# Performance work log

Hardware: AMD Instinct MI355X
Metric: run time of the kernel (lower is better)

Reference implementation:

```python
import jax, jax.numpy as jnp
import numpy as np

LOG2PI = float(np.log(2.0 * np.pi))
EPS_SHIFT = -0.5   # self.eps
TAU = 0.5          # self.tau
ETA = 1.0          # self.eta
MAG_A = 5500.0     # magnitude remap constants from forward()
MAG_B = 1100.0


def setup_inputs() -> dict:
    key = jax.random.key(0)
    k1, k2, k3, k4, k5 = jax.random.split(key, 5)
    B, K, C = 4096, 128, 64
    z = jax.random.normal(k1, (B, K, 2), dtype=jnp.float32)
    # per-keypoint mixture weights summing to 1 (GMM weights_)
    weights = jax.nn.softmax(jax.random.normal(k2, (K, C), dtype=jnp.float32), axis=-1)
    means = jax.random.normal(k3, (K, C, 2), dtype=jnp.float32)
    # SPD covariances: A A^T + 0.2 I
    A = jax.random.normal(k4, (K, C, 2, 2), dtype=jnp.float32) * 0.3
    covs = jnp.einsum('kcij,kclj->kcil', A, A) + 0.2 * jnp.eye(2, dtype=jnp.float32)
    # latent_stats unnormalization factor per latent coordinate (2/(max-min))
    scale = jax.random.uniform(k5, (K, 2), dtype=jnp.float32, minval=0.5, maxval=2.0)
    return {"z": z, "weights": weights, "means": means, "covs": covs, "scale": scale}


def _gmm_pdf_and_grad(z, weights, means, covs):
    # z: [B,K,2]  weights: [K,C]  means: [K,C,2]  covs: [K,C,2,2]
    a = covs[..., 0, 0]; b = covs[..., 0, 1]
    c = covs[..., 1, 0]; d = covs[..., 1, 1]
    det = a * d - b * c                                  # [K,C]
    inv00 = d / det; inv01 = -b / det
    inv10 = -c / det; inv11 = a / det
    diff = z[:, :, None, :] - means[None]                # [B,K,C,2]
    d0 = diff[..., 0]; d1 = diff[..., 1]
    s0 = inv00 * d0 + inv01 * d1                         # Sigma^{-1} diff, [B,K,C]
    s1 = inv10 * d0 + inv11 * d1
    maha = d0 * s0 + d1 * s1                             # [B,K,C]
    logp = -0.5 * (maha + jnp.log(det) + 2.0 * LOG2PI)   # MVN log_prob (D=2)
    comp = weights[None] * jnp.exp(logp)                 # weighted component densities
    pdf = comp.sum(-1)                                   # [B,K]
    # analytic grad of pdf wrt z: sum_c comp_c * (-Sigma_c^{-1} (z-mu_c))
    g0 = -(comp * s0).sum(-1)
    g1 = -(comp * s1).sum(-1)
    grad = jnp.stack([g0, g1], axis=-1)                  # [B,K,2]
    return pdf, grad


def reference(z, weights, means, covs, scale):
    B, K, _ = z.shape
    pdf, grad = _gmm_pdf_and_grad(z, weights, means, covs)
    # densities duplicated per coordinate: [pdf_i, pdf_i] per keypoint -> [B, 2K]
    densities = jnp.repeat(pdf, 2, axis=-1)
    density_norm = jax.nn.sigmoid((densities + EPS_SHIFT) / TAU)
    # unnormalize_gradient: elementwise rescale into raw latent space
    grad_raw = grad * scale[None]                        # [B,K,2]
    nrm = jnp.linalg.norm(grad_raw, axis=-1, keepdims=True)  # [B,K,1]
    mag = jnp.exp((-nrm + MAG_A) / MAG_B)
    negexp_grad = (grad_raw / nrm) * mag                 # [B,K,2]
    return density_norm, ETA * negexp_grad.reshape(B, 2 * K)
```

## Files before the change

### kernel.cpp

```cpp
#include <hip/hip_runtime.h>

#define K_KP   128
#define C_COMP 64
#define TK     8
#define TBS    32
#define NB     4
#define LDS_STRIDE 388

typedef float v2f __attribute__((ext_vector_type(2)));

#if __has_builtin(__builtin_amdgcn_exp2f)
#define EXP2F(x) __builtin_amdgcn_exp2f(x)
#else
#define EXP2F(x) exp2f(x)
#endif
#if __has_builtin(__builtin_amdgcn_logf)
#define LOG2F_(x) __builtin_amdgcn_logf(x)
#else
#define LOG2F_(x) __log2f(x)
#endif
#if __has_builtin(__builtin_amdgcn_rcpf)
#define RCPF(x) __builtin_amdgcn_rcpf(x)
#else
#define RCPF(x) (1.0f/(x))
#endif
#if __has_builtin(__builtin_amdgcn_rsqf)
#define RSQF(x) __builtin_amdgcn_rsqf(x)
#else
#define RSQF(x) rsqrtf(x)
#endif

#define EVAL(m0, m1, i00, i01, i11, lc, ZX, ZY, PDF, G0, G1)            \
    {                                                                   \
        v2f d0 = ZX - (m0);                                             \
        v2f d1 = ZY - (m1);                                             \
        v2f s0 = (i00) * d0 + (i01) * d1;   \
        v2f s1 = (i01) * d0 + (i11) * d1;                               \
        v2f arg = (lc) - d0 * s0 - d1 * s1;           \
        v2f e;                                                          \
        e.x = EXP2F(arg.x);                                             \
        e.y = EXP2F(arg.y);                                             \
        PDF += e;                                                       \
        G0 += e * s0;                                                   \
        G1 += e * s1;                                                   \
    }

__global__ __launch_bounds__(256, 4) void recovery_kernel(
    const float* __restrict__ z,
    const float* __restrict__ weights,
    const float* __restrict__ means,
    const float* __restrict__ covs,
    const float* __restrict__ scale,
    float* __restrict__ out, int B)
{
    __shared__ float lds[TK * LDS_STRIDE];

    const int t  = threadIdx.x;
    const int kb = blockIdx.x & 15;
    const int bb = blockIdx.x >> 4;
    const int k0 = kb * TK;
    const int b0 = bb * (TBS * NB);

    const float K2       = 0.72134752044f;
    const float LOG2_2PI = 2.6514961295f;
    for (int i = t; i < TK * C_COMP; i += 256) {
        int kl = i >> 6;
        int c  = i & 63;
        int g  = (k0 + kl) * C_COMP + c;
        float w  = weights[g];
        float m0 = means[2*g], m1 = means[2*g + 1];
        float a  = covs[4*g],     bq = covs[4*g + 1];
        float cq = covs[4*g + 2], d  = covs[4*g + 3];
        float det  = a*d - bq*cq;
        float rdet = RCPF(det);
        float i00 = d  * rdet * K2;
        float i01 = -bq * rdet * K2;
        float i11 = a  * rdet * K2;
        float lc = LOG2F_(w) - LOG2_2PI - 0.5f * LOG2F_(det);
        float* row = &lds[kl * LDS_STRIDE + (c >> 1) * 12];
        ((float4*)(row + (c & 1) * 4))[0] = make_float4(m0, m1, i00, i01);
        ((float2*)(row + 8 + (c & 1) * 2))[0] = make_float2(i11, lc);
    }
    __syncthreads();

    const int kl = t & 7;
    const int bl = t >> 3;
    const int kg = k0 + kl;

    const float2* z2 = (const float2*)z;
    float zx[NB], zy[NB];
#pragma unroll
    for (int j = 0; j < NB; ++j) {
        int b = b0 + bl + j * TBS;
        float2 v = z2[(size_t)b * K_KP + kg];
        zx[j] = v.x; zy[j] = v.y;
    }

    v2f ZXa = {zx[0], zx[1]}, ZXb = {zx[2], zx[3]};
    v2f ZYa = {zy[0], zy[1]}, ZYb = {zy[2], zy[3]};
    v2f pdfa = {0.f, 0.f}, pdfb = {0.f, 0.f};
    v2f g0a  = {0.f, 0.f}, g0b  = {0.f, 0.f};
    v2f g1a  = {0.f, 0.f}, g1b  = {0.f, 0.f};

    const float* kp = &lds[kl * LDS_STRIDE];
#pragma unroll 4
    for (int p = 0; p < C_COMP / 2; ++p) {
        float4 A0 = *(const float4*)(kp + p * 12);
        float4 A1 = *(const float4*)(kp + p * 12 + 4);
        float4 Bp = *(const float4*)(kp + p * 12 + 8);
        EVAL(A0.x, A0.y, A0.z, A0.w, Bp.x, Bp.y, ZXa, ZYa, pdfa, g0a, g1a);
        EVAL(A0.x, A0.y, A0.z, A0.w, Bp.x, Bp.y, ZXb, ZYb, pdfb, g0b, g1b);
        EVAL(A1.x, A1.y, A1.z, A1.w, Bp.z, Bp.w, ZXa, ZYa, pdfa, g0a, g1a);
        EVAL(A1.x, A1.y, A1.z, A1.w, Bp.z, Bp.w, ZXb, ZYb, pdfb, g0b, g1b);
    }

    float pdf[NB] = {pdfa.x, pdfa.y, pdfb.x, pdfb.y};
    float gs0[NB] = {g0a.x, g0a.y, g0b.x, g0b.y};
    float gs1[NB] = {g1a.x, g1a.y, g1b.x, g1b.y};

    float2 sc = ((const float2*)scale)[kg];
    const float NEG_INV_K2 = -1.3862943611f;
    float f0 = sc.x * NEG_INV_K2;
    float f1 = sc.y * NEG_INV_K2;
    const int KK2 = 2 * K_KP;
    float* out0 = out;
    float* out1 = out + (size_t)B * KK2;
#pragma unroll
    for (int j = 0; j < NB; ++j) {
        int b = b0 + bl + j * TBS;
        float x  = 2.0f * pdf[j] - 1.0f;
        float ex = EXP2F(-1.44269504f * x);
        float dn = RCPF(1.0f + ex);
        float g0 = gs0[j] * f0;
        float g1 = gs1[j] * f1;
        float n2 = fmaf(g0, g0, g1 * g1);
        float rn = RSQF(n2);
        float nrm = n2 * rn;
        float mag = EXP2F(fmaf(nrm, -0.0013115409f, 7.2134752044f));
        float m = rn * mag;
        ((float2*)(out0 + (size_t)b * KK2 + 2 * kg))[0] = make_float2(dn, dn);
        ((float2*)(out1 + (size_t)b * KK2 + 2 * kg))[0] = make_float2(g0 * m, g1 * m);
    }
}

extern "C" void kernel_launch(void* const* d_in, const int* in_sizes, int n_in,
                              void* d_out, int out_size, void* d_ws, size_t ws_size,
                              hipStream_t stream) {
    const float* z       = (const float*)d_in[0];
    const float* weights = (const float*)d_in[1];
    const float* means   = (const float*)d_in[2];
    const float* covs    = (const float*)d_in[3];
    const float* scale   = (const float*)d_in[4];
    float* out = (float*)d_out;

    int B = in_sizes[0] / (2 * K_KP);
    int grid = (K_KP / TK) * (B / (TBS * NB));
    recovery_kernel<<<grid, 256, 0, stream>>>(z, weights, means, covs, scale, out, B);
}
```

Before: 74.68 us.

## Broadcast GMM component params via readlane instead of LDS staging

Each wavefront now owns one keypoint. Its 64 lanes each precompute one mixture component's parameters in registers, and v_readlane broadcasts them as scalars inside the unrolled component loop. This removes the LDS tile, the __syncthreads barrier and the per-component LDS loads. Block indices are also swizzled to change the order in which blocks are scheduled. The cost is that each thread now handles 2 batch rows instead of 4, and the loop needs many readlane ops that may serialize on the scalar path.

```diff
diff --git a/kernel.cpp b/kernel.cpp
--- a/kernel.cpp
+++ b/kernel.cpp
@@ -2,10 +2,7 @@
 
 #define K_KP   128
 #define C_COMP 64
-#define TK     8
-#define TBS    32
-#define NB     4
-#define LDS_STRIDE 388
+#define KPB    4
 
 typedef float v2f __attribute__((ext_vector_type(2)));
 
@@ -30,7 +27,13 @@
 #define RSQF(x) rsqrtf(x)
 #endif
 
-#define EVAL(m0, m1, i00, i01, i11, lc, ZX, ZY, PDF, G0, G1)            \
+__device__ __forceinline__ float rlane(float v, int l) {
+    union { float f; int i; } u; u.f = v;
+    u.i = __builtin_amdgcn_readlane(u.i, l);
+    return u.f;
+}
+
+#define EVAL(m0, m1, i00, i01, i11, lc)                                 \
     {                                                                   \
         v2f d0 = ZX - (m0);                                             \
         v2f d1 = ZY - (m1);                                             \
@@ -40,9 +43,9 @@
         v2f e;                                                          \
         e.x = EXP2F(arg.x);                                             \
         e.y = EXP2F(arg.y);                                             \
-        PDF += e;                                                       \
-        G0 += e * s0;                                                   \
-        G1 += e * s1;                                                   \
+        pdf += e;                                                       \
+        G0  += e * s0;                                                  \
+        G1  += e * s1;                                                  \
     }
 
 __global__ __launch_bounds__(256, 4) void recovery_kernel(
@@ -53,93 +56,76 @@
     const float* __restrict__ scale,
     float* __restrict__ out, int B)
 {
-    __shared__ float lds[TK * LDS_STRIDE];
+    const int t    = threadIdx.x;
+    const int lane = t & 63;
+    const int wv   = __builtin_amdgcn_readfirstlane(t >> 6);
 
-    const int t  = threadIdx.x;
-    const int kb = blockIdx.x & 15;
-    const int bb = blockIdx.x >> 4;
-    const int k0 = kb * TK;
-    const int b0 = bb * (TBS * NB);
+    const int bid = blockIdx.x;
+    const int swz = (bid & 7) * 128 + (bid >> 3);
+    const int kb  = swz & 31;
+    const int bb  = swz >> 5;
+    const int k   = kb * KPB + wv;
+    const int b0  = bb * 128;
 
     const float K2       = 0.72134752044f;
     const float LOG2_2PI = 2.6514961295f;
-    for (int i = t; i < TK * C_COMP; i += 256) {
-        int kl = i >> 6;
-        int c  = i & 63;
-        int g  = (k0 + kl) * C_COMP + c;
-        float w  = weights[g];
-        float m0 = means[2*g], m1 = means[2*g + 1];
-        float a  = covs[4*g],     bq = covs[4*g + 1];
-        float cq = covs[4*g + 2], d  = covs[4*g + 3];
-        float det  = a*d - bq*cq;
-        float rdet = RCPF(det);
-        float i00 = d  * rdet * K2;
-        float i01 = -bq * rdet * K2;
-        float i11 = a  * rdet * K2;
-        float lc = LOG2F_(w) - LOG2_2PI - 0.5f * LOG2F_(det);
-        float* row = &lds[kl * LDS_STRIDE + (c >> 1) * 12];
-        ((float4*)(row + (c & 1) * 4))[0] = make_float4(m0, m1, i00, i01);
-        ((float2*)(row + 8 + (c & 1) * 2))[0] = make_float2(i11, lc);
-    }
-    __syncthreads();
-
-    const int kl = t & 7;
-    const int bl = t >> 3;
-    const int kg = k0 + kl;
+    const int g = k * C_COMP + lane;
+    float  w  = weights[g];
+    float2 m  = ((const float2*)means)[g];
+    float4 cv = ((const float4*)covs)[g];
+    float det  = cv.x * cv.w - cv.y * cv.z;
+    float rdet = RCPF(det);
+    float vm0  = m.x;
+    float vm1  = m.y;
+    float vi00 =  cv.w * rdet * K2;
+    float vi01 = -cv.y * rdet * K2;
+    float vi11 =  cv.x * rdet * K2;
+    float vlc  = LOG2F_(w) - LOG2_2PI - 0.5f * LOG2F_(det);
 
     const float2* z2 = (const float2*)z;
-    float zx[NB], zy[NB];
+    float2 za = z2[(size_t)(b0 + lane)      * K_KP + k];
+    float2 zb = z2[(size_t)(b0 + lane + 64) * K_KP + k];
+    v2f ZX = {za.x, zb.x};
+    v2f ZY = {za.y, zb.y};
+    v2f pdf = {0.f, 0.f}, G0 = {0.f, 0.f}, G1 = {0.f, 0.f};
+
 #pragma unroll
-    for (int j = 0; j < NB; ++j) {
-        int b = b0 + bl + j * TBS;
-        float2 v = z2[(size_t)b * K_KP + kg];
-        zx[j] = v.x; zy[j] = v.y;
+    for (int c = 0; c < C_COMP; ++c) {
+        float m0  = rlane(vm0, c);
+        float m1  = rlane(vm1, c);
+        float i00 = rlane(vi00, c);
+        float i01 = rlane(vi01, c);
+        float i11 = rlane(vi11, c);
+        float lc  = rlane(vlc, c);
+        EVAL(m0, m1, i00, i01, i11, lc);
     }
 
-    v2f ZXa = {zx[0], zx[1]}, ZXb = {zx[2], zx[3]};
-    v2f ZYa = {zy[0], zy[1]}, ZYb = {zy[2], zy[3]};
-    v2f pdfa = {0.f, 0.f}, pdfb = {0.f, 0.f};
-    v2f g0a  = {0.f, 0.f}, g0b  = {0.f, 0.f};
-    v2f g1a  = {0.f, 0.f}, g1b  = {0.f, 0.f};
-
-    const float* kp = &lds[kl * LDS_STRIDE];
-#pragma unroll 4
-    for (int p = 0; p < C_COMP / 2; ++p) {
-        float4 A0 = *(const float4*)(kp + p * 12);
-        float4 A1 = *(const float4*)(kp + p * 12 + 4);
-        float4 Bp = *(const float4*)(kp + p * 12 + 8);
-        EVAL(A0.x, A0.y, A0.z, A0.w, Bp.x, Bp.y, ZXa, ZYa, pdfa, g0a, g1a);
-        EVAL(A0.x, A0.y, A0.z, A0.w, Bp.x, Bp.y, ZXb, ZYb, pdfb, g0b, g1b);
-        EVAL(A1.x, A1.y, A1.z, A1.w, Bp.z, Bp.w, ZXa, ZYa, pdfa, g0a, g1a);
-        EVAL(A1.x, A1.y, A1.z, A1.w, Bp.z, Bp.w, ZXb, ZYb, pdfb, g0b, g1b);
-    }
-
-    float pdf[NB] = {pdfa.x, pdfa.y, pdfb.x, pdfb.y};
-    float gs0[NB] = {g0a.x, g0a.y, g0b.x, g0b.y};
-    float gs1[NB] = {g1a.x, g1a.y, g1b.x, g1b.y};
-
-    float2 sc = ((const float2*)scale)[kg];
+    float2 sc = ((const float2*)scale)[k];
     const float NEG_INV_K2 = -1.3862943611f;
     float f0 = sc.x * NEG_INV_K2;
     float f1 = sc.y * NEG_INV_K2;
     const int KK2 = 2 * K_KP;
     float* out0 = out;
     float* out1 = out + (size_t)B * KK2;
+
+    float pdfj[2] = {pdf.x, pdf.y};
+    float gs0j[2] = {G0.x, G0.y};
+    float gs1j[2] = {G1.x, G1.y};
 #pragma unroll
-    for (int j = 0; j < NB; ++j) {
-        int b = b0 + bl + j * TBS;
-        float x  = 2.0f * pdf[j] - 1.0f;
+    for (int j = 0; j < 2; ++j) {
+        int b = b0 + lane + j * 64;
+        float x  = 2.0f * pdfj[j] - 1.0f;
         float ex = EXP2F(-1.44269504f * x);
         float dn = RCPF(1.0f + ex);
-        float g0 = gs0[j] * f0;
-        float g1 = gs1[j] * f1;
+        float g0 = gs0j[j] * f0;
+        float g1 = gs1j[j] * f1;
         float n2 = fmaf(g0, g0, g1 * g1);
         float rn = RSQF(n2);
         float nrm = n2 * rn;
         float mag = EXP2F(fmaf(nrm, -0.0013115409f, 7.2134752044f));
-        float m = rn * mag;
-        ((float2*)(out0 + (size_t)b * KK2 + 2 * kg))[0] = make_float2(dn, dn);
-        ((float2*)(out1 + (size_t)b * KK2 + 2 * kg))[0] = make_float2(g0 * m, g1 * m);
+        float mm = rn * mag;
+        ((float2*)(out0 + (size_t)b * KK2 + 2 * k))[0] = make_float2(dn, dn);
+        ((float2*)(out1 + (size_t)b * KK2 + 2 * k))[0] = make_float2(g0 * mm, g1 * mm);
     }
 }
 
@@ -154,6 +140,6 @@
     float* out = (float*)d_out;
 
     int B = in_sizes[0] / (2 * K_KP);
-    int grid = (K_KP / TK) * (B / (TBS * NB));
+    int grid = (K_KP / KPB) * (B / 128);
     recovery_kernel<<<grid, 256, 0, stream>>>(z, weights, means, covs, scale, out, B);
 }
```

After: 77.28 us. +3.5%, slower.
